# Kernel tuning notes

Hardware: AMD Instinct MI355X
Metric: run time of the kernel (lower is better)

## Reference

```python
import jax, jax.numpy as jnp
import numpy as np

B, S = 2, 1024
D, L, HD, H, KV, F, E, K, V = 1024, 2, 64, 16, 4, 2048, 8, 2, 32000
EPS = 1e-5
THETA = 1e6
REP = H // KV


def setup_inputs() -> dict:
    key = jax.random.key(0)
    ks = jax.random.split(key, 12)
    w = lambda k, shape: jax.random.normal(k, shape, jnp.float32) * 0.02
    return {
        'input_ids': jax.random.randint(ks[0], (B, S), 0, V, jnp.int32),
        'positions': jnp.arange(S),
        'tok_emb': w(ks[1], (V, D)),
        'attn_norm_w': jnp.ones((L, D), jnp.float32),
        'ffn_norm_w': jnp.ones((L, D), jnp.float32),
        'wq': w(ks[2], (L, D, H * HD)),
        'wk': w(ks[3], (L, D, KV * HD)),
        'wv': w(ks[4], (L, D, KV * HD)),
        'wo': w(ks[5], (L, H * HD, D)),
        'gate_w': w(ks[6], (L, D, E)),
        'w1': w(ks[7], (L, E, D, F)),
        'w2': w(ks[8], (L, E, F, D)),
        'w3': w(ks[9], (L, E, D, F)),
        'final_norm_w': jnp.ones((D,), jnp.float32),
        'out_w': w(ks[10], (D, V)),
    }


def rmsnorm(x, w):
    x32 = x.astype(jnp.float32)
    n = x32 * jax.lax.rsqrt(jnp.mean(x32 * x32, axis=-1, keepdims=True) + EPS)
    return n.astype(x.dtype) * w


def rope(x, cos, sin):
    # x: [B, S, h, HD]; cos/sin: [S, HD//2]; pairs are interleaved (even, odd)
    xe, xo = x[..., 0::2], x[..., 1::2]
    c, s = cos[None, :, None, :], sin[None, :, None, :]
    re = xe * c - xo * s
    im = xe * s + xo * c
    return jnp.stack([re, im], axis=-1).reshape(x.shape)


def attention(x, cos, sin, mask, wq_l, wk_l, wv_l, wo_l):
    q = (x @ wq_l).reshape(B, S, H, HD)
    k = (x @ wk_l).reshape(B, S, KV, HD)
    v = (x @ wv_l).reshape(B, S, KV, HD)
    q, k = rope(q, cos, sin), rope(k, cos, sin)
    k = jnp.repeat(k, REP, axis=2)  # GQA: repeat_interleave kv heads
    v = jnp.repeat(v, REP, axis=2)
    scale = HD ** -0.5
    scores = jnp.einsum('bqhd,bkhd->bhqk', q, k) * scale + mask[None, None]
    p = jax.nn.softmax(scores.astype(jnp.float32), axis=-1).astype(q.dtype)
    o = jnp.einsum('bhqk,bkhd->bqhd', p, v).reshape(B, S, H * HD)
    return o @ wo_l


def moe(x, gate_l, w1_l, w2_l, w3_l):
    xs = x.reshape(-1, D)  # [N, D]
    N = xs.shape[0]
    logits = xs @ gate_l  # [N, E]
    topw, sel = jax.lax.top_k(logits, K)
    topw = jax.nn.softmax(topw.astype(jnp.float32), axis=1).astype(x.dtype)
    comb = jnp.zeros((N, E), x.dtype).at[jnp.arange(N)[:, None], sel].add(topw)
    h1 = jax.nn.silu(jnp.einsum('nd,edf->nef', xs, w1_l))
    h3 = jnp.einsum('nd,edf->nef', xs, w3_l)
    y = jnp.einsum('nef,efd->ned', h1 * h3, w2_l)
    return jnp.einsum('ned,ne->nd', y, comb).reshape(x.shape)


def reference(input_ids, positions, tok_emb, attn_norm_w, ffn_norm_w, wq, wk, wv, wo,
              gate_w, w1, w2, w3, final_norm_w, out_w):
    freqs = 1.0 / (THETA ** (jnp.arange(0, HD, 2, dtype=jnp.float32) / HD))  # [HD//2]
    ang = positions.astype(jnp.float32)[:, None] * freqs[None, :]  # [S, HD//2]
    cos, sin = jnp.cos(ang), jnp.sin(ang)
    mask = jnp.triu(jnp.full((S, S), -1e9, jnp.float32), 1)  # causal
    h = tok_emb[input_ids]  # [B, S, D]
    for l in range(L):
        h = h + attention(rmsnorm(h, attn_norm_w[l]), cos, sin, mask, wq[l], wk[l], wv[l], wo[l])
        h = h + moe(rmsnorm(h, ffn_norm_w[l]), gate_w[l], w1[l], w2[l], w3[l])
    return rmsnorm(h, final_norm_w) @ out_w  # [B, S, V]
```

## Files before the change

kernel.cpp:

```cpp
#include <hip/hip_runtime.h>
#include <math.h>

typedef unsigned short ushort_t;
typedef __attribute__((ext_vector_type(8))) short short8;
typedef __attribute__((ext_vector_type(4))) float f32x4;

#define Bq 2
#define Sq 1024
#define Dq 1024
#define Lq 2
#define HDq 64
#define Hq 16
#define KVq 4
#define Fq 2048
#define Eq 8
#define TOPK 2
#define Vq 32000
#define Nq (Bq*Sq)
#define EPSq 1e-5f
#define MROW (Nq*TOPK)

__device__ __forceinline__ float b2f(ushort_t u) {
  return __uint_as_float(((unsigned int)u) << 16);
}
__device__ __forceinline__ ushort_t f2b(float f) {
  unsigned int u = __float_as_uint(f);
  u += 0x7fffu + ((u >> 16) & 1u);
  return (ushort_t)(u >> 16);
}

typedef const void __attribute__((address_space(1)))* gas_cptr;
typedef void __attribute__((address_space(3)))* las_ptr;
__device__ __forceinline__ void gload16(const void* g, void* l) {
  __builtin_amdgcn_global_load_lds((gas_cptr)g, (las_ptr)l, 16, 0, 0);
}

__device__ __forceinline__ void xcd_tiles(int &bx, int &by) {
  int gx = gridDim.x;
  int nwg = gx * gridDim.y;
  int bid = blockIdx.y * gx + blockIdx.x;
  int q8 = nwg >> 3, r8 = nwg & 7;
  int xcd = bid & 7, idx = bid >> 3;
  int swz = (xcd < r8) ? xcd * (q8 + 1) + idx
                       : r8 * (q8 + 1) + (xcd - r8) * q8 + idx;
  bx = swz % gx;
  by = swz / gx;
}

#define MF ((size_t)1024*1024)
#define O_H    ((size_t)0)
#define O_XH   (2*MF)
#define O_XL   (3*MF)
#define O_QKV  (4*MF)
#define O_ATH  (7*MF)
#define O_ATL  (8*MF)
#define O_QH   (9*MF)
#define O_QL   (10*MF)
#define O_KH   (11*MF)
#define O_KL   (11*MF + MF/4)
#define O_VTH  (11*MF + MF/2)
#define O_VTL  (11*MF + 3*MF/4)
#define O_COS  (12*MF)
#define O_SIN  (O_COS + 32768)
#define O_LOG  (O_SIN + 32768)
#define O_TPW  (O_LOG + 16384)
#define O_WTH  (O_COS + MF/8)
#define O_WTL  (O_WTH + MF/2)
#define O_SC   (27*MF/2)
#define O_XGH  (4*MF)
#define O_XGL  (6*MF)
#define O_HB   (O_SC)
#define O_H13H (O_SC + 16*MF)
#define O_H13L (O_SC + 20*MF)
#define O_Y    (O_SC + 24*MF)
#define O_INT  (42*MF)


__global__ void k_rope_table(const int* __restrict__ pos, float* __restrict__ cosT,
                             float* __restrict__ sinT) {
  int i = blockIdx.x * blockDim.x + threadIdx.x;
  if (i >= Sq * 32) return;
  int s = i >> 5, f = i & 31;
  float freq = 1.0f / powf(1.0e6f, (float)f / 32.0f);
  float ang = (float)pos[s] * freq;
  cosT[i] = cosf(ang);
  sinT[i] = sinf(ang);
}

__global__ void k_embed(const int* __restrict__ ids, const float* __restrict__ emb,
                        float* __restrict__ h) {
  int n = blockIdx.x;
  const float4* src = (const float4*)(emb + (size_t)ids[n] * Dq);
  float4* dst = (float4*)(h + (size_t)n * Dq);
  dst[threadIdx.x] = src[threadIdx.x];
}

__global__ void k_rmsnorm3(const float* __restrict__ in, const float* __restrict__ w,
                           ushort_t* __restrict__ outh, ushort_t* __restrict__ outl) {
  int n = blockIdx.x;
  int t = threadIdx.x;
  float4 v = ((const float4*)(in + (size_t)n * Dq))[t];
  float ss = v.x*v.x + v.y*v.y + v.z*v.z + v.w*v.w;
  #pragma unroll
  for (int o = 32; o > 0; o >>= 1) ss += __shfl_down(ss, o);
  __shared__ float red[4];
  if ((t & 63) == 0) red[t >> 6] = ss;
  __syncthreads();
  float tot = red[0] + red[1] + red[2] + red[3];
  float r = rsqrtf(tot / (float)Dq + EPSq);
  float4 wl = ((const float4*)w)[t];
  float o4[4];
  o4[0] = v.x * r * wl.x; o4[1] = v.y * r * wl.y;
  o4[2] = v.z * r * wl.z; o4[3] = v.w * r * wl.w;
  ushort_t* oh = outh + (size_t)n * Dq + t * 4;
  ushort_t* ol = outl + (size_t)n * Dq + t * 4;
  #pragma unroll
  for (int j = 0; j < 4; j++) {
    ushort_t hi = f2b(o4[j]);
    oh[j] = hi;
    ol[j] = f2b(o4[j] - b2f(hi));
  }
}

__global__ void k_rope3(const float* __restrict__ qkv, const float* __restrict__ cosT,
                        const float* __restrict__ sinT,
                        ushort_t* __restrict__ qh, ushort_t* __restrict__ ql,
                        ushort_t* __restrict__ kh, ushort_t* __restrict__ kl) {
  int i = blockIdx.x * blockDim.x + threadIdx.x;
  int n = i / 640, r = i % 640;
  int hh = r >> 5, f = r & 31;
  int s = n & (Sq - 1);
  float c = cosT[s * 32 + f], sn = sinT[s * 32 + f];
  int srcCol = (hh < 16) ? hh * 64 + 2 * f : 1024 + (hh - 16) * 64 + 2 * f;
  const float* pp = qkv + (size_t)n * 1536 + srcCol;
  float xe = pp[0], xo = pp[1];
  float re = xe * c - xo * sn;
  float im = xe * sn + xo * c;
  ushort_t reh = f2b(re), imh = f2b(im);
  ushort_t rel = f2b(re - b2f(reh)), iml = f2b(im - b2f(imh));
  if (hh < 16) {
    size_t d = (size_t)n * 1024 + hh * 64 + 2 * f;
    qh[d] = reh; qh[d + 1] = imh;
    ql[d] = rel; ql[d + 1] = iml;
  } else {
    size_t d = (size_t)n * 256 + (hh - 16) * 64 + 2 * f;
    kh[d] = reh; kh[d + 1] = imh;
    kl[d] = rel; kl[d + 1] = iml;
  }
}

__global__ void k_convT2(const float* __restrict__ src, ushort_t* __restrict__ dh,
                         ushort_t* __restrict__ dl, int srcStride, int dstStride,
                         int zdiv, long long srcZa, long long srcZb, long long dstZ) {
  __shared__ float tile[32][33];
  int z = blockIdx.z;
  const float* s = src + (long long)(z / zdiv) * srcZa + (long long)(z % zdiv) * srcZb;
  int r0 = blockIdx.y * 32, c0 = blockIdx.x * 32;
  int tc = threadIdx.x & 31, tr = threadIdx.x >> 5;
  #pragma unroll
  for (int i = 0; i < 4; ++i)
    tile[tr + i * 8][tc] = s[(long long)(r0 + tr + i * 8) * srcStride + c0 + tc];
  __syncthreads();
  #pragma unroll
  for (int i = 0; i < 4; ++i) {
    float v = tile[tc][tr + i * 8];
    ushort_t hi = f2b(v);
    long long idx = (long long)z * dstZ + (long long)(c0 + tr + i * 8) * dstStride + r0 + tc;
    dh[idx] = hi;
    if (dl) dl[idx] = f2b(v - b2f(hi));
  }
}

__global__ __launch_bounds__(256)
void k_mgemm3(const ushort_t* __restrict__ Ah, const ushort_t* __restrict__ Al,
              const ushort_t* __restrict__ Bh, const ushort_t* __restrict__ Bl,
              float* __restrict__ C,
              int N, int Kd, int lda, int ldc,
              int outmode, int mode,
              const int* __restrict__ grpBase, const int* __restrict__ grpCnt, int M) {
  __shared__ alignas(16) short Ash[128 * 64];
  __shared__ alignas(16) short Asl[128 * 64];
  __shared__ alignas(16) short Bsh[128 * 64];
  __shared__ alignas(16) short Bsl[128 * 64];
  int z = blockIdx.z;
  const ushort_t *Abh, *Abl, *Bbh, *Bbl;
  long long cOff;
  int Me = M;
  if (mode == 1) {
    int base = grpBase[z];
    Me = grpCnt[z];
    Abh = Ah + (long long)base * lda;
    Abl = Al + (long long)base * lda;
    long long bo = (long long)z * ((long long)N * Kd);
    Bbh = Bh + bo; Bbl = Bl + bo;
    cOff = (long long)base * ldc;
  } else {
    Abh = Ah; Abl = Al; Bbh = Bh; Bbl = Bl; cOff = 0;
  }
  int bx, by;
  xcd_tiles(bx, by);
  int m0 = bx * 128, n0 = by * 128;
  if (m0 >= Me) return;
  int t = threadIdx.x, w = t >> 6, lane = t & 63;
  int wm = w >> 1, wn = w & 1;
  int rA = lane >> 3;
  int sOff = ((lane & 7) ^ rA) << 3;
  f32x4 acc[4][4];
  #pragma unroll
  for (int i = 0; i < 4; ++i)
    #pragma unroll
    for (int j = 0; j < 4; ++j) { acc[i][j].x = 0.f; acc[i][j].y = 0.f; acc[i][j].z = 0.f; acc[i][j].w = 0.f; }
  int nkt = Kd >> 6;
  for (int kt = 0; kt < nkt; ++kt) {
    int k0 = kt << 6;
    #pragma unroll
    for (int i = 0; i < 4; ++i) {
      int j = (w << 2) + i;
      int row = (j << 3) + rA;
      long long ao = (long long)(m0 + row) * lda + k0 + sOff;
      long long bo = (long long)(n0 + row) * Kd + k0 + sOff;
      gload16(Abh + ao, &Ash[j * 512]);
      gload16(Abl + ao, &Asl[j * 512]);
      gload16(Bbh + bo, &Bsh[j * 512]);
      gload16(Bbl + bo, &Bsl[j * 512]);
    }
    __syncthreads();
    #pragma unroll
    for (int kk = 0; kk < 2; ++kk) {
      short8 afh[4], afl[4], bfh[4], bfl[4];
      int cl = (kk << 2) + (lane >> 4);
      #pragma unroll
      for (int mi = 0; mi < 4; ++mi) {
        int row = (wm << 6) + (mi << 4) + (lane & 15);
        int idx = (row << 6) + ((cl ^ (row & 7)) << 3);
        afh[mi] = *(const short8*)&Ash[idx];
        afl[mi] = *(const short8*)&Asl[idx];
      }
      #pragma unroll
      for (int nj = 0; nj < 4; ++nj) {
        int row = (wn << 6) + (nj << 4) + (lane & 15);
        int idx = (row << 6) + ((cl ^ (row & 7)) << 3);
        bfh[nj] = *(const short8*)&Bsh[idx];
        bfl[nj] = *(const short8*)&Bsl[idx];
      }
      #pragma unroll
      for (int mi = 0; mi < 4; ++mi)
        #pragma unroll
        for (int nj = 0; nj < 4; ++nj) {
          acc[mi][nj] = __builtin_amdgcn_mfma_f32_16x16x32_bf16(afh[mi], bfh[nj], acc[mi][nj], 0, 0, 0);
          acc[mi][nj] = __builtin_amdgcn_mfma_f32_16x16x32_bf16(afl[mi], bfh[nj], acc[mi][nj], 0, 0, 0);
          acc[mi][nj] = __builtin_amdgcn_mfma_f32_16x16x32_bf16(afh[mi], bfl[nj], acc[mi][nj], 0, 0, 0);
        }
    }
    __syncthreads();
  }
  #pragma unroll
  for (int mi = 0; mi < 4; ++mi) {
    #pragma unroll
    for (int nj = 0; nj < 4; ++nj) {
      int col = n0 + (wn << 6) + (nj << 4) + (lane & 15);
      if (col >= N) continue;
      #pragma unroll
      for (int r = 0; r < 4; ++r) {
        int lr = m0 + (wm << 6) + (mi << 4) + (lane >> 4) * 4 + r;
        if (lr >= Me) continue;
        long long ci = cOff + (long long)lr * ldc + col;
        float v = ((float*)&acc[mi][nj])[r];
        if (outmode == 0) C[ci] = v;
        else C[ci] += v;
      }
    }
  }
}

__global__ __launch_bounds__(256)
void k_mgemm1(const ushort_t* __restrict__ Ah, const ushort_t* __restrict__ Bh,
              float* __restrict__ C,
              int N, int Kd, int lda, int ldc,
              int outmode, int mode,
              const int* __restrict__ grpBase, const int* __restrict__ grpCnt, int M) {
  __shared__ alignas(16) short Ash[2][128 * 64];
  __shared__ alignas(16) short Bsh[2][128 * 64];
  int z = blockIdx.z;
  const ushort_t *Abh, *Bbh;
  long long cOff;
  int Me = M;
  if (mode == 1) {
    int base = grpBase[z];
    Me = grpCnt[z];
    Abh = Ah + (long long)base * lda;
    Bbh = Bh + (long long)z * ((long long)N * Kd);
    cOff = (long long)base * ldc;
  } else {
    Abh = Ah; Bbh = Bh; cOff = 0;
  }
  int bx, by;
  xcd_tiles(bx, by);
  int m0 = bx * 128, n0 = by * 128;
  if (m0 >= Me) return;
  int t = threadIdx.x, w = t >> 6, lane = t & 63;
  int wm = w >> 1, wn = w & 1;
  int rA = lane >> 3;
  int sOff = ((lane & 7) ^ rA) << 3;
  f32x4 acc[4][4];
  #pragma unroll
  for (int i = 0; i < 4; ++i)
    #pragma unroll
    for (int j = 0; j < 4; ++j) { acc[i][j].x = 0.f; acc[i][j].y = 0.f; acc[i][j].z = 0.f; acc[i][j].w = 0.f; }
  int nkt = Kd >> 6;
  #pragma unroll
  for (int i = 0; i < 4; ++i) {
    int j = (w << 2) + i;
    int row = (j << 3) + rA;
    gload16(Abh + (long long)(m0 + row) * lda + sOff, &Ash[0][j * 512]);
    gload16(Bbh + (long long)(n0 + row) * Kd + sOff, &Bsh[0][j * 512]);
  }
  __syncthreads();
  int cur = 0;
  for (int kt = 0; kt < nkt; ++kt) {
    if (kt + 1 < nkt) {
      int k0 = (kt + 1) << 6;
      #pragma unroll
      for (int i = 0; i < 4; ++i) {
        int j = (w << 2) + i;
        int row = (j << 3) + rA;
        gload16(Abh + (long long)(m0 + row) * lda + k0 + sOff, &Ash[cur ^ 1][j * 512]);
        gload16(Bbh + (long long)(n0 + row) * Kd + k0 + sOff, &Bsh[cur ^ 1][j * 512]);
      }
    }
    #pragma unroll
    for (int kk = 0; kk < 2; ++kk) {
      short8 afh[4], bfh[4];
      int cl = (kk << 2) + (lane >> 4);
      #pragma unroll
      for (int mi = 0; mi < 4; ++mi) {
        int row = (wm << 6) + (mi << 4) + (lane & 15);
        afh[mi] = *(const short8*)&Ash[cur][(row << 6) + ((cl ^ (row & 7)) << 3)];
      }
      #pragma unroll
      for (int nj = 0; nj < 4; ++nj) {
        int row = (wn << 6) + (nj << 4) + (lane & 15);
        bfh[nj] = *(const short8*)&Bsh[cur][(row << 6) + ((cl ^ (row & 7)) << 3)];
      }
      #pragma unroll
      for (int mi = 0; mi < 4; ++mi)
        #pragma unroll
        for (int nj = 0; nj < 4; ++nj)
          acc[mi][nj] = __builtin_amdgcn_mfma_f32_16x16x32_bf16(afh[mi], bfh[nj], acc[mi][nj], 0, 0, 0);
    }
    __syncthreads();
    cur ^= 1;
  }
  #pragma unroll
  for (int mi = 0; mi < 4; ++mi) {
    #pragma unroll
    for (int nj = 0; nj < 4; ++nj) {
      int col = n0 + (wn << 6) + (nj << 4) + (lane & 15);
      if (col >= N) continue;
      #pragma unroll
      for (int r = 0; r < 4; ++r) {
        int lr = m0 + (wm << 6) + (mi << 4) + (lane >> 4) * 4 + r;
        if (lr >= Me) continue;
        long long ci = cOff + (long long)lr * ldc + col;
        float v = ((float*)&acc[mi][nj])[r];
        if (outmode == 0) C[ci] = v;
        else C[ci] += v;
      }
    }
  }
}

__global__ __launch_bounds__(256)
void k_qk3(const ushort_t* __restrict__ qh, const ushort_t* __restrict__ ql,
           const ushort_t* __restrict__ kh, const ushort_t* __restrict__ kl,
           float* __restrict__ sc) {
  __shared__ alignas(16) short Ash[128 * 64];
  __shared__ alignas(16) short Asl[128 * 64];
  __shared__ alignas(16) short Bsh[128 * 64];
  __shared__ alignas(16) short Bsl[128 * 64];
  int zl = blockIdx.z;
  int b = zl >> 4, hh = zl & 15, kv = hh >> 2;
  int m0 = blockIdx.x * 128, n0 = blockIdx.y * 128;
  if (n0 > m0 + 127) return;
  long long aBase = ((long long)(b * Sq) * Hq + hh) * HDq;
  long long bBase = ((long long)(b * Sq) * KVq + kv) * HDq;
  int t = threadIdx.x, w = t >> 6, lane = t & 63;
  int wm = w >> 1, wn = w & 1;
  int rA = lane >> 3;
  int sOff = ((lane & 7) ^ rA) << 3;
  f32x4 acc[4][4];
  #pragma unroll
  for (int i = 0; i < 4; ++i)
    #pragma unroll
    for (int j = 0; j < 4; ++j) { acc[i][j].x = 0.f; acc[i][j].y = 0.f; acc[i][j].z = 0.f; acc[i][j].w = 0.f; }
  {
    #pragma unroll
    for (int i = 0; i < 4; ++i) {
      int j = (w << 2) + i;
      int row = (j << 3) + rA;
      long long ao = aBase + (long long)(m0 + row) * (Hq * HDq) + sOff;
      long long bo = bBase + (long long)(n0 + row) * (KVq * HDq) + sOff;
      gload16(qh + ao, &Ash[j * 512]);
      gload16(ql + ao, &Asl[j * 512]);
      gload16(kh + bo, &Bsh[j * 512]);
      gload16(kl + bo, &Bsl[j * 512]);
    }
    __syncthreads();
    #pragma unroll
    for (int kk = 0; kk < 2; ++kk) {
      short8 afh[4], afl[4], bfh[4], bfl[4];
      int cl = (kk << 2) + (lane >> 4);
      #pragma unroll
      for (int mi = 0; mi < 4; ++mi) {
        int row = (wm << 6) + (mi << 4) + (lane & 15);
        int idx = (row << 6) + ((cl ^ (row & 7)) << 3);
        afh[mi] = *(const short8*)&Ash[idx];
        afl[mi] = *(const short8*)&Asl[idx];
      }
      #pragma unroll
      for (int nj = 0; nj < 4; ++nj) {
        int row = (wn << 6) + (nj << 4) + (lane & 15);
        int idx = (row << 6) + ((cl ^ (row & 7)) << 3);
        bfh[nj] = *(const short8*)&Bsh[idx];
        bfl[nj] = *(const short8*)&Bsl[idx];
      }
      #pragma unroll
      for (int mi = 0; mi < 4; ++mi)
        #pragma unroll
        for (int nj = 0; nj < 4; ++nj) {
          acc[mi][nj] = __builtin_amdgcn_mfma_f32_16x16x32_bf16(afh[mi], bfh[nj], acc[mi][nj], 0, 0, 0);
          acc[mi][nj] = __builtin_amdgcn_mfma_f32_16x16x32_bf16(afl[mi], bfh[nj], acc[mi][nj], 0, 0, 0);
          acc[mi][nj] = __builtin_amdgcn_mfma_f32_16x16x32_bf16(afh[mi], bfl[nj], acc[mi][nj], 0, 0, 0);
        }
    }
  }
  float* out = sc + (long long)zl * Sq * Sq;
  #pragma unroll
  for (int mi = 0; mi < 4; ++mi) {
    #pragma unroll
    for (int nj = 0; nj < 4; ++nj) {
      int col = n0 + (wn << 6) + (nj << 4) + (lane & 15);
      #pragma unroll
      for (int r = 0; r < 4; ++r) {
        int lr = m0 + (wm << 6) + (mi << 4) + (lane >> 4) * 4 + r;
        out[(long long)lr * Sq + col] = ((float*)&acc[mi][nj])[r] * 0.125f;
      }
    }
  }
}

__global__ __launch_bounds__(256)
void k_softmax3(const float* __restrict__ sc, ushort_t* __restrict__ ph,
                ushort_t* __restrict__ pl) {
  int row = blockIdx.x * 4 + (threadIdx.x >> 6);
  int lane = threadIdx.x & 63;
  int qi = row & (Sq - 1);
  const float* p = sc + (long long)row * Sq;
  float vals[16];
  float mx = -3.0e38f;
  #pragma unroll
  for (int j = 0; j < 16; j++) {
    int idx = lane + j * 64;
    float v = (idx <= qi) ? p[idx] : -3.0e38f;
    vals[j] = v;
    mx = fmaxf(mx, v);
  }
  #pragma unroll
  for (int o = 32; o > 0; o >>= 1) mx = fmaxf(mx, __shfl_xor(mx, o));
  float sum = 0.0f;
  #pragma unroll
  for (int j = 0; j < 16; j++) {
    int idx = lane + j * 64;
    float e = (idx <= qi) ? expf(vals[j] - mx) : 0.0f;
    vals[j] = e;
    sum += e;
  }
  #pragma unroll
  for (int o = 32; o > 0; o >>= 1) sum += __shfl_xor(sum, o);
  float inv = 1.0f / sum;
  long long base = (long long)row * Sq;
  #pragma unroll
  for (int j = 0; j < 16; j++) {
    int idx = lane + j * 64;
    float pr = vals[j] * inv;
    ushort_t hi = f2b(pr);
    ph[base + idx] = hi;
    pl[base + idx] = f2b(pr - b2f(hi));
  }
}

__global__ __launch_bounds__(256)
void k_pv3(const ushort_t* __restrict__ ph, const ushort_t* __restrict__ pl,
           const ushort_t* __restrict__ vth, const ushort_t* __restrict__ vtl,
           ushort_t* __restrict__ ath, ushort_t* __restrict__ atl) {
  __shared__ alignas(16) short Ash[128 * 64];
  __shared__ alignas(16) short Asl[128 * 64];
  __shared__ alignas(16) short Bsh[128 * 64];
  __shared__ alignas(16) short Bsl[128 * 64];
  int zl = blockIdx.z;
  int b = zl >> 4, hh = zl & 15, kv = hh >> 2;
  int m0 = blockIdx.x * 128;
  const ushort_t* Abh = ph + (long long)zl * Sq * Sq;
  const ushort_t* Abl = pl + (long long)zl * Sq * Sq;
  const ushort_t* Bbh = vth + (long long)((b * KVq + kv) * HDq) * Sq;
  const ushort_t* Bbl = vtl + (long long)((b * KVq + kv) * HDq) * Sq;
  int t = threadIdx.x, w = t >> 6, lane = t & 63;
  int wm = w >> 1, wn = w & 1;
  int rA = lane >> 3;
  int sOff = ((lane & 7) ^ rA) << 3;
  f32x4 acc[4][4];
  #pragma unroll
  for (int i = 0; i < 4; ++i)
    #pragma unroll
    for (int j = 0; j < 4; ++j) { acc[i][j].x = 0.f; acc[i][j].y = 0.f; acc[i][j].z = 0.f; acc[i][j].w = 0.f; }
  int ktmax = 2 * blockIdx.x + 2;
  for (int kt = 0; kt < ktmax; ++kt) {
    int k0 = kt << 6;
    #pragma unroll
    for (int i = 0; i < 4; ++i) {
      int j = (w << 2) + i;
      int row = (j << 3) + rA;
      long long ao = (long long)(m0 + row) * Sq + k0 + sOff;
      long long bo = (long long)(row & 63) * Sq + k0 + sOff;
      gload16(Abh + ao, &Ash[j * 512]);
      gload16(Abl + ao, &Asl[j * 512]);
      gload16(Bbh + bo, &Bsh[j * 512]);
      gload16(Bbl + bo, &Bsl[j * 512]);
    }
    __syncthreads();
    #pragma unroll
    for (int kk = 0; kk < 2; ++kk) {
      short8 afh[4], afl[4], bfh[4], bfl[4];
      int cl = (kk << 2) + (lane >> 4);
      #pragma unroll
      for (int mi = 0; mi < 4; ++mi) {
        int row = (wm << 6) + (mi << 4) + (lane & 15);
        int idx = (row << 6) + ((cl ^ (row & 7)) << 3);
        afh[mi] = *(const short8*)&Ash[idx];
        afl[mi] = *(const short8*)&Asl[idx];
      }
      #pragma unroll
      for (int nj = 0; nj < 4; ++nj) {
        int row = (wn << 6) + (nj << 4) + (lane & 15);
        int idx = (row << 6) + ((cl ^ (row & 7)) << 3);
        bfh[nj] = *(const short8*)&Bsh[idx];
        bfl[nj] = *(const short8*)&Bsl[idx];
      }
      #pragma unroll
      for (int mi = 0; mi < 4; ++mi)
        #pragma unroll
        for (int nj = 0; nj < 4; ++nj) {
          acc[mi][nj] = __builtin_amdgcn_mfma_f32_16x16x32_bf16(afh[mi], bfh[nj], acc[mi][nj], 0, 0, 0);
          acc[mi][nj] = __builtin_amdgcn_mfma_f32_16x16x32_bf16(afl[mi], bfh[nj], acc[mi][nj], 0, 0, 0);
          acc[mi][nj] = __builtin_amdgcn_mfma_f32_16x16x32_bf16(afh[mi], bfl[nj], acc[mi][nj], 0, 0, 0);
        }
    }
    __syncthreads();
  }
  #pragma unroll
  for (int mi = 0; mi < 4; ++mi) {
    #pragma unroll
    for (int nj = 0; nj < 4; ++nj) {
      int col = (wn << 6) + (nj << 4) + (lane & 15);
      if (col >= HDq) continue;
      #pragma unroll
      for (int r = 0; r < 4; ++r) {
        int lr = m0 + (wm << 6) + (mi << 4) + (lane >> 4) * 4 + r;
        long long ci = ((long long)(b * Sq + lr)) * (Hq * HDq) + hh * HDq + col;
        float v = ((float*)&acc[mi][nj])[r];
        ushort_t hi = f2b(v);
        ath[ci] = hi;
        atl[ci] = f2b(v - b2f(hi));
      }
    }
  }
}

__global__ void k_gate(const ushort_t* __restrict__ xh, const ushort_t* __restrict__ xl,
                       const float* __restrict__ gw, float* __restrict__ logits) {
  int n = blockIdx.x * 4 + (threadIdx.x >> 6);
  int lane = threadIdx.x & 63;
  float acc[Eq];
  #pragma unroll
  for (int e = 0; e < Eq; e++) acc[e] = 0.0f;
  for (int d = lane; d < Dq; d += 64) {
    size_t idx = (size_t)n * Dq + d;
    float xv = b2f(xh[idx]) + b2f(xl[idx]);
    const float* g = gw + (size_t)d * Eq;
    #pragma unroll
    for (int e = 0; e < Eq; e++) acc[e] += xv * g[e];
  }
  #pragma unroll
  for (int o = 32; o > 0; o >>= 1)
    #pragma unroll
    for (int e = 0; e < Eq; e++) acc[e] += __shfl_xor(acc[e], o);
  if (lane == 0) {
    #pragma unroll
    for (int e = 0; e < Eq; e++) logits[(size_t)n * Eq + e] = acc[e];
  }
}

__global__ void k_zero_counts(int* c) { if (threadIdx.x < 16) c[threadIdx.x] = 0; }

__global__ void k_route_count(const float* __restrict__ logits, float* __restrict__ topw,
                              int* __restrict__ sel, int* __restrict__ counts) {
  int n = blockIdx.x * blockDim.x + threadIdx.x;
  if (n >= Nq) return;
  const float* lg = logits + (size_t)n * Eq;
  int i1 = 0; float v1 = lg[0];
  #pragma unroll
  for (int e = 1; e < Eq; e++) if (lg[e] > v1) { v1 = lg[e]; i1 = e; }
  int i2 = -1; float v2 = -3.0e38f;
  #pragma unroll
  for (int e = 0; e < Eq; e++) if (e != i1 && lg[e] > v2) { v2 = lg[e]; i2 = e; }
  float e2 = expf(v2 - v1);
  float s = 1.0f + e2;
  topw[n * 2 + 0] = 1.0f / s;
  topw[n * 2 + 1] = e2 / s;
  sel[n * 2 + 0] = i1;
  sel[n * 2 + 1] = i2;
  atomicAdd(&counts[i1], 1);
  atomicAdd(&counts[i2], 1);
}

__global__ void k_scan(const int* __restrict__ counts, int* __restrict__ bases,
                       int* __restrict__ counts2) {
  if (threadIdx.x == 0) {
    int s = 0;
    for (int e = 0; e < Eq; e++) { bases[e] = s; s += counts[e]; counts2[e] = 0; }
  }
}

__global__ void k_route_assign(const int* __restrict__ sel, int* __restrict__ counts2,
                               const int* __restrict__ bases, int* __restrict__ row2tok,
                               int* __restrict__ posof) {
  int n = blockIdx.x * blockDim.x + threadIdx.x;
  if (n >= Nq) return;
  #pragma unroll
  for (int slot = 0; slot < TOPK; slot++) {
    int e = sel[n * 2 + slot];
    int pos = atomicAdd(&counts2[e], 1);
    int row = bases[e] + pos;
    row2tok[row] = n;
    posof[n * 2 + slot] = row;
  }
}

__global__ void k_gather_us(const ushort_t* __restrict__ xh, const ushort_t* __restrict__ xl,
                            const int* __restrict__ row2tok,
                            ushort_t* __restrict__ xgh, ushort_t* __restrict__ xgl) {
  int row = blockIdx.x;
  int tok = row2tok[row];
  int t = threadIdx.x;
  const uint2* sh = (const uint2*)(xh + (size_t)tok * Dq);
  const uint2* sl = (const uint2*)(xl + (size_t)tok * Dq);
  ((uint2*)(xgh + (size_t)row * Dq))[t] = sh[t];
  ((uint2*)(xgl + (size_t)row * Dq))[t] = sl[t];
}

__global__ void k_silumul3b(const float* __restrict__ hb,
                            ushort_t* __restrict__ oh, ushort_t* __restrict__ ol) {
  long total = (long)MROW * Fq;
  long i = (long)blockIdx.x * blockDim.x + threadIdx.x;
  long st = (long)gridDim.x * blockDim.x;
  for (; i < total; i += st) {
    long r = i >> 11, f = i & 2047;
    float a = hb[(r << 12) + f];
    float b = hb[(r << 12) + 2048 + f];
    float s = (a / (1.0f + expf(-a))) * b;
    ushort_t hi = f2b(s);
    oh[i] = hi;
    ol[i] = f2b(s - b2f(hi));
  }
}

__global__ void k_moe_combine(float* __restrict__ h, const float* __restrict__ y,
                              const float* __restrict__ topw, const int* __restrict__ posof) {
  int n = blockIdx.x;
  int t = threadIdx.x;
  float w0 = topw[n * 2 + 0], w1 = topw[n * 2 + 1];
  int r0 = posof[n * 2 + 0], r1 = posof[n * 2 + 1];
  float4 a = ((const float4*)(y + (size_t)r0 * Dq))[t];
  float4 b = ((const float4*)(y + (size_t)r1 * Dq))[t];
  float4 hv = ((float4*)(h + (size_t)n * Dq))[t];
  hv.x += w0 * a.x + w1 * b.x;
  hv.y += w0 * a.y + w1 * b.y;
  hv.z += w0 * a.z + w1 * b.z;
  hv.w += w0 * a.w + w1 * b.w;
  ((float4*)(h + (size_t)n * Dq))[t] = hv;
}

extern "C" void kernel_launch(void* const* d_in, const int* in_sizes, int n_in,
                              void* d_out, int out_size, void* d_ws, size_t ws_size,
                              hipStream_t stream) {
  const int* ids       = (const int*)d_in[0];
  const int* pos       = (const int*)d_in[1];
  const float* tok_emb = (const float*)d_in[2];
  const float* attn_nw = (const float*)d_in[3];
  const float* ffn_nw  = (const float*)d_in[4];
  const float* wq      = (const float*)d_in[5];
  const float* wk      = (const float*)d_in[6];
  const float* wv      = (const float*)d_in[7];
  const float* wo      = (const float*)d_in[8];
  const float* gate    = (const float*)d_in[9];
  const float* w1      = (const float*)d_in[10];
  const float* w2      = (const float*)d_in[11];
  const float* w3      = (const float*)d_in[12];
  const float* fnw     = (const float*)d_in[13];
  const float* outw    = (const float*)d_in[14];
  float* out = (float*)d_out;
  float* ws = (float*)d_ws;
  float* dws = out;

  float* h      = ws + O_H;
  ushort_t* xh  = (ushort_t*)(ws + O_XH);
  ushort_t* xl  = (ushort_t*)(ws + O_XL);
  float* qkv    = ws + O_QKV;
  ushort_t* ath = (ushort_t*)(ws + O_ATH);
  ushort_t* atl = (ushort_t*)(ws + O_ATL);
  ushort_t* qhB = (ushort_t*)(ws + O_QH);
  ushort_t* qlB = (ushort_t*)(ws + O_QL);
  ushort_t* khB = (ushort_t*)(ws + O_KH);
  ushort_t* klB = (ushort_t*)(ws + O_KL);
  ushort_t* vth = (ushort_t*)(ws + O_VTH);
  ushort_t* vtl = (ushort_t*)(ws + O_VTL);
  float* cosT   = ws + O_COS;
  float* sinT   = ws + O_SIN;
  float* logits = ws + O_LOG;
  float* topw   = ws + O_TPW;
  ushort_t* wTh = (ushort_t*)(ws + O_WTH);
  ushort_t* wTl = (ushort_t*)(ws + O_WTL);
  float* sc     = dws;
  ushort_t* ph  = (ushort_t*)(dws + 32*MF);
  ushort_t* pl  = (ushort_t*)(ws + O_SC);
  ushort_t* wQh = (ushort_t*)dws;
  ushort_t* wQl = (ushort_t*)(dws + MF);
  ushort_t* xgh = (ushort_t*)(ws + O_XGH);
  ushort_t* xgl = (ushort_t*)(ws + O_XGL);
  ushort_t* wAh = (ushort_t*)dws;
  ushort_t* wAl = (ushort_t*)(dws + 16*MF);
  float* hb     = ws + O_HB;
  ushort_t* h13h= (ushort_t*)(ws + O_H13H);
  ushort_t* h13l= (ushort_t*)(ws + O_H13L);
  float* y      = ws + O_Y;
  ushort_t* owTh= (ushort_t*)(ws + O_SC);
  int* ip = (int*)(ws + O_INT);
  int* counts  = ip;
  int* counts2 = ip + 8;
  int* bases   = ip + 16;
  int* sel     = ip + 32;
  int* row2tok = ip + 32 + 4096;
  int* posof   = ip + 32 + 8192;

  k_rope_table<<<128, 256, 0, stream>>>(pos, cosT, sinT);
  k_embed<<<Nq, 256, 0, stream>>>(ids, tok_emb, h);

  for (int l = 0; l < Lq; l++) {
    k_rmsnorm3<<<Nq, 256, 0, stream>>>(h, attn_nw + (size_t)l * Dq, xh, xl);
    k_convT2<<<dim3(32, 32, 1), 256, 0, stream>>>(wq + (long long)l*Dq*Hq*HDq, wQh, wQl, Hq*HDq, Dq, 1, 0, 0, 0);
    k_convT2<<<dim3(8, 32, 1), 256, 0, stream>>>(wk + (long long)l*Dq*KVq*HDq, wQh + (size_t)1024*1024, wQl + (size_t)1024*1024, KVq*HDq, Dq, 1, 0, 0, 0);
    k_convT2<<<dim3(8, 32, 1), 256, 0, stream>>>(wv + (long long)l*Dq*KVq*HDq, wQh + (size_t)1280*1024, wQl + (size_t)1280*1024, KVq*HDq, Dq, 1, 0, 0, 0);
    k_mgemm3<<<dim3(16, 12, 1), 256, 0, stream>>>(xh, xl, wQh, wQl, qkv, 1536, Dq, Dq, 1536, 0, 0, nullptr, nullptr, Nq);
    k_rope3<<<(Nq * 20 * 32) / 256, 256, 0, stream>>>(qkv, cosT, sinT, qhB, qlB, khB, klB);
    k_convT2<<<dim3(2, 32, Bq*KVq), 256, 0, stream>>>(qkv + 1280, vth, vtl, 1536, Sq,
           KVq, (long long)Sq*1536, HDq, (long long)HDq*Sq);
    k_qk3<<<dim3(8, 8, 32), 256, 0, stream>>>(qhB, qlB, khB, klB, sc);
    k_softmax3<<<(32 * Sq) / 4, 256, 0, stream>>>(sc, ph, pl);
    k_pv3<<<dim3(8, 1, 32), 256, 0, stream>>>(ph, pl, vth, vtl, ath, atl);
    k_convT2<<<dim3(32, 32, 1), 256, 0, stream>>>(wo + (long long)l*Hq*HDq*Dq, wTh, wTl, Dq, Hq*HDq, 1, 0, 0, 0);
    k_mgemm3<<<dim3(16, 8, 1), 256, 0, stream>>>(ath, atl, wTh, wTl, h, Dq, Hq*HDq, Hq*HDq, Dq, 1, 0, nullptr, nullptr, Nq);

    k_rmsnorm3<<<Nq, 256, 0, stream>>>(h, ffn_nw + (size_t)l * Dq, xh, xl);
    k_gate<<<Nq / 4, 256, 0, stream>>>(xh, xl, gate + (size_t)l * Dq * Eq, logits);
    k_zero_counts<<<1, 32, 0, stream>>>(counts);
    k_route_count<<<Nq / 256, 256, 0, stream>>>(logits, topw, sel, counts);
    k_scan<<<1, 1, 0, stream>>>(counts, bases, counts2);
    k_route_assign<<<Nq / 256, 256, 0, stream>>>(sel, counts2, bases, row2tok, posof);
    k_gather_us<<<MROW, 256, 0, stream>>>(xh, xl, row2tok, xgh, xgl);
    int last = (l == Lq - 1);
    k_convT2<<<dim3(64, 32, 8), 256, 0, stream>>>(w1 + (long long)l*Eq*Dq*Fq, wAh, last ? nullptr : wAl,
           Fq, Dq, 1, (long long)Dq*Fq, 0, (long long)4096*1024);
    k_convT2<<<dim3(64, 32, 8), 256, 0, stream>>>(w3 + (long long)l*Eq*Dq*Fq,
           wAh + (size_t)2048*1024, last ? nullptr : (wAl + (size_t)2048*1024),
           Fq, Dq, 1, (long long)Dq*Fq, 0, (long long)4096*1024);
    if (last) k_mgemm1<<<dim3(16, 32, 8), 256, 0, stream>>>(xgh, wAh, hb, 4096, Dq, Dq, 4096, 0, 1, bases, counts, 0);
    else      k_mgemm3<<<dim3(16, 32, 8), 256, 0, stream>>>(xgh, xgl, wAh, wAl, hb, 4096, Dq, Dq, 4096, 0, 1, bases, counts, 0);
    k_silumul3b<<<4096, 256, 0, stream>>>(hb, h13h, h13l);
    k_convT2<<<dim3(32, 64, 8), 256, 0, stream>>>(w2 + (long long)l*Eq*Fq*Dq, wAh, last ? nullptr : wAl,
           Dq, Fq, 1, (long long)Fq*Dq, 0, (long long)Dq*Fq);
    if (last) k_mgemm1<<<dim3(16, 8, 8), 256, 0, stream>>>(h13h, wAh, y, Dq, Fq, Fq, Dq, 0, 1, bases, counts, 0);
    else      k_mgemm3<<<dim3(16, 8, 8), 256, 0, stream>>>(h13h, h13l, wAh, wAl, y, Dq, Fq, Fq, Dq, 0, 1, bases, counts, 0);
    k_moe_combine<<<Nq, 256, 0, stream>>>(h, y, topw, posof);
  }

  k_rmsnorm3<<<Nq, 256, 0, stream>>>(h, fnw, xh, xl);
  k_convT2<<<dim3(1000, 32, 1), 256, 0, stream>>>(outw, owTh, nullptr, Vq, Dq, 1, 0, 0, 0);
  k_mgemm1<<<dim3(16, 250, 1), 256, 0, stream>>>(xh, owTh, out, Vq, Dq, Dq, Vq, 0, 0, nullptr, nullptr, Nq);
}
```

Measured before the change: 1.451 ms.

## Fuse SiLU-gate multiply into MoE up-projection epilogue and double-buffer PV kernel

The w1 and w3 weights are interleaved row-wise during transposition, so each adjacent output column pair holds the gate and up values. The grouped GEMM epilogue then uses a lane shuffle to compute silu(a)*b and writes the bf16 hi/lo split directly. This removes the fp32 intermediate buffer and the separate silumul kernel. Separately, the attention PV kernel gains double-buffered shared-memory tile loads to overlap global loads with MFMA work, at the cost of twice the LDS use, which may lower occupancy.

```diff
diff --git a/kernel.cpp b/kernel.cpp
--- a/kernel.cpp
+++ b/kernel.cpp
@@ -69,7 +69,6 @@
 #define O_SC   (27*MF/2)
 #define O_XGH  (4*MF)
 #define O_XGL  (6*MF)
-#define O_HB   (O_SC)
 #define O_H13H (O_SC + 16*MF)
 #define O_H13L (O_SC + 20*MF)
 #define O_Y    (O_SC + 24*MF)
@@ -151,7 +150,8 @@
 
 __global__ void k_convT2(const float* __restrict__ src, ushort_t* __restrict__ dh,
                          ushort_t* __restrict__ dl, int srcStride, int dstStride,
-                         int zdiv, long long srcZa, long long srcZb, long long dstZ) {
+                         int zdiv, long long srcZa, long long srcZb, long long dstZ,
+                         int rowScale, int rowOff) {
   __shared__ float tile[32][33];
   int z = blockIdx.z;
   const float* s = src + (long long)(z / zdiv) * srcZa + (long long)(z % zdiv) * srcZb;
@@ -165,7 +165,8 @@
   for (int i = 0; i < 4; ++i) {
     float v = tile[tc][tr + i * 8];
     ushort_t hi = f2b(v);
-    long long idx = (long long)z * dstZ + (long long)(c0 + tr + i * 8) * dstStride + r0 + tc;
+    long long drow = (long long)(c0 + tr + i * 8) * rowScale + rowOff;
+    long long idx = (long long)z * dstZ + drow * dstStride + r0 + tc;
     dh[idx] = hi;
     if (dl) dl[idx] = f2b(v - b2f(hi));
   }
@@ -175,6 +176,7 @@
 void k_mgemm3(const ushort_t* __restrict__ Ah, const ushort_t* __restrict__ Al,
               const ushort_t* __restrict__ Bh, const ushort_t* __restrict__ Bl,
               float* __restrict__ C,
+              ushort_t* __restrict__ Ch2, ushort_t* __restrict__ Cl2,
               int N, int Kd, int lda, int ldc,
               int outmode, int mode,
               const int* __restrict__ grpBase, const int* __restrict__ grpCnt, int M) {
@@ -184,7 +186,7 @@
   __shared__ alignas(16) short Bsl[128 * 64];
   int z = blockIdx.z;
   const ushort_t *Abh, *Abl, *Bbh, *Bbl;
-  long long cOff;
+  long long cOff, cOff2;
   int Me = M;
   if (mode == 1) {
     int base = grpBase[z];
@@ -194,8 +196,9 @@
     long long bo = (long long)z * ((long long)N * Kd);
     Bbh = Bh + bo; Bbl = Bl + bo;
     cOff = (long long)base * ldc;
+    cOff2 = (long long)base * 2048;
   } else {
-    Abh = Ah; Abl = Al; Bbh = Bh; Bbl = Bl; cOff = 0;
+    Abh = Ah; Abl = Al; Bbh = Bh; Bbl = Bl; cOff = 0; cOff2 = 0;
   }
   int bx, by;
   xcd_tiles(bx, by);
@@ -259,15 +262,21 @@
     #pragma unroll
     for (int nj = 0; nj < 4; ++nj) {
       int col = n0 + (wn << 6) + (nj << 4) + (lane & 15);
-      if (col >= N) continue;
       #pragma unroll
       for (int r = 0; r < 4; ++r) {
         int lr = m0 + (wm << 6) + (mi << 4) + (lane >> 4) * 4 + r;
-        if (lr >= Me) continue;
-        long long ci = cOff + (long long)lr * ldc + col;
         float v = ((float*)&acc[mi][nj])[r];
-        if (outmode == 0) C[ci] = v;
-        else C[ci] += v;
+        float pv = __shfl_xor(v, 1);
+        if (col >= N || lr >= Me) continue;
+        if (outmode == 0) C[cOff + (long long)lr * ldc + col] = v;
+        else if (outmode == 1) C[cOff + (long long)lr * ldc + col] += v;
+        else if (!(lane & 1)) {
+          float s = (v / (1.0f + expf(-v))) * pv;
+          long long ci2 = cOff2 + (long long)lr * 2048 + (col >> 1);
+          ushort_t hi = f2b(s);
+          Ch2[ci2] = hi;
+          Cl2[ci2] = f2b(s - b2f(hi));
+        }
       }
     }
   }
@@ -276,6 +285,7 @@
 __global__ __launch_bounds__(256)
 void k_mgemm1(const ushort_t* __restrict__ Ah, const ushort_t* __restrict__ Bh,
               float* __restrict__ C,
+              ushort_t* __restrict__ Ch2, ushort_t* __restrict__ Cl2,
               int N, int Kd, int lda, int ldc,
               int outmode, int mode,
               const int* __restrict__ grpBase, const int* __restrict__ grpCnt, int M) {
@@ -283,7 +293,7 @@
   __shared__ alignas(16) short Bsh[2][128 * 64];
   int z = blockIdx.z;
   const ushort_t *Abh, *Bbh;
-  long long cOff;
+  long long cOff, cOff2;
   int Me = M;
   if (mode == 1) {
     int base = grpBase[z];
@@ -291,8 +301,9 @@
     Abh = Ah + (long long)base * lda;
     Bbh = Bh + (long long)z * ((long long)N * Kd);
     cOff = (long long)base * ldc;
+    cOff2 = (long long)base * 2048;
   } else {
-    Abh = Ah; Bbh = Bh; cOff = 0;
+    Abh = Ah; Bbh = Bh; cOff = 0; cOff2 = 0;
   }
   int bx, by;
   xcd_tiles(bx, by);
@@ -356,15 +367,21 @@
     #pragma unroll
     for (int nj = 0; nj < 4; ++nj) {
       int col = n0 + (wn << 6) + (nj << 4) + (lane & 15);
-      if (col >= N) continue;
       #pragma unroll
       for (int r = 0; r < 4; ++r) {
         int lr = m0 + (wm << 6) + (mi << 4) + (lane >> 4) * 4 + r;
-        if (lr >= Me) continue;
-        long long ci = cOff + (long long)lr * ldc + col;
         float v = ((float*)&acc[mi][nj])[r];
-        if (outmode == 0) C[ci] = v;
-        else C[ci] += v;
+        float pv = __shfl_xor(v, 1);
+        if (col >= N || lr >= Me) continue;
+        if (outmode == 0) C[cOff + (long long)lr * ldc + col] = v;
+        else if (outmode == 1) C[cOff + (long long)lr * ldc + col] += v;
+        else if (!(lane & 1)) {
+          float s = (v / (1.0f + expf(-v))) * pv;
+          long long ci2 = cOff2 + (long long)lr * 2048 + (col >> 1);
+          ushort_t hi = f2b(s);
+          Ch2[ci2] = hi;
+          Cl2[ci2] = f2b(s - b2f(hi));
+        }
       }
     }
   }
@@ -493,10 +510,10 @@
 void k_pv3(const ushort_t* __restrict__ ph, const ushort_t* __restrict__ pl,
            const ushort_t* __restrict__ vth, const ushort_t* __restrict__ vtl,
            ushort_t* __restrict__ ath, ushort_t* __restrict__ atl) {
-  __shared__ alignas(16) short Ash[128 * 64];
-  __shared__ alignas(16) short Asl[128 * 64];
-  __shared__ alignas(16) short Bsh[128 * 64];
-  __shared__ alignas(16) short Bsl[128 * 64];
+  __shared__ alignas(16) short Ash[2][128 * 64];
+  __shared__ alignas(16) short Asl[2][128 * 64];
+  __shared__ alignas(16) short Bsh[2][128 * 64];
+  __shared__ alignas(16) short Bsl[2][128 * 64];
   int zl = blockIdx.z;
   int b = zl >> 4, hh = zl & 15, kv = hh >> 2;
   int m0 = blockIdx.x * 128;
@@ -514,20 +531,34 @@
     #pragma unroll
     for (int j = 0; j < 4; ++j) { acc[i][j].x = 0.f; acc[i][j].y = 0.f; acc[i][j].z = 0.f; acc[i][j].w = 0.f; }
   int ktmax = 2 * blockIdx.x + 2;
+  #pragma unroll
+  for (int i = 0; i < 4; ++i) {
+    int j = (w << 2) + i;
+    int row = (j << 3) + rA;
+    long long ao = (long long)(m0 + row) * Sq + sOff;
+    long long bo = (long long)(row & 63) * Sq + sOff;
+    gload16(Abh + ao, &Ash[0][j * 512]);
+    gload16(Abl + ao, &Asl[0][j * 512]);
+    gload16(Bbh + bo, &Bsh[0][j * 512]);
+    gload16(Bbl + bo, &Bsl[0][j * 512]);
+  }
+  __syncthreads();
+  int cur = 0;
   for (int kt = 0; kt < ktmax; ++kt) {
-    int k0 = kt << 6;
-    #pragma unroll
-    for (int i = 0; i < 4; ++i) {
-      int j = (w << 2) + i;
-      int row = (j << 3) + rA;
-      long long ao = (long long)(m0 + row) * Sq + k0 + sOff;
-      long long bo = (long long)(row & 63) * Sq + k0 + sOff;
-      gload16(Abh + ao, &Ash[j * 512]);
-      gload16(Abl + ao, &Asl[j * 512]);
-      gload16(Bbh + bo, &Bsh[j * 512]);
-      gload16(Bbl + bo, &Bsl[j * 512]);
-    }
-    __syncthreads();
+    if (kt + 1 < ktmax) {
+      int k0 = (kt + 1) << 6;
+      #pragma unroll
+      for (int i = 0; i < 4; ++i) {
+        int j = (w << 2) + i;
+        int row = (j << 3) + rA;
+        long long ao = (long long)(m0 + row) * Sq + k0 + sOff;
+        long long bo = (long long)(row & 63) * Sq + k0 + sOff;
+        gload16(Abh + ao, &Ash[cur ^ 1][j * 512]);
+        gload16(Abl + ao, &Asl[cur ^ 1][j * 512]);
+        gload16(Bbh + bo, &Bsh[cur ^ 1][j * 512]);
+        gload16(Bbl + bo, &Bsl[cur ^ 1][j * 512]);
+      }
+    }
     #pragma unroll
     for (int kk = 0; kk < 2; ++kk) {
       short8 afh[4], afl[4], bfh[4], bfl[4];
@@ -536,15 +567,15 @@
       for (int mi = 0; mi < 4; ++mi) {
         int row = (wm << 6) + (mi << 4) + (lane & 15);
         int idx = (row << 6) + ((cl ^ (row & 7)) << 3);
-        afh[mi] = *(const short8*)&Ash[idx];
-        afl[mi] = *(const short8*)&Asl[idx];
+        afh[mi] = *(const short8*)&Ash[cur][idx];
+        afl[mi] = *(const short8*)&Asl[cur][idx];
       }
       #pragma unroll
       for (int nj = 0; nj < 4; ++nj) {
         int row = (wn << 6) + (nj << 4) + (lane & 15);
         int idx = (row << 6) + ((cl ^ (row & 7)) << 3);
-        bfh[nj] = *(const short8*)&Bsh[idx];
-        bfl[nj] = *(const short8*)&Bsl[idx];
+        bfh[nj] = *(const short8*)&Bsh[cur][idx];
+        bfl[nj] = *(const short8*)&Bsl[cur][idx];
       }
       #pragma unroll
       for (int mi = 0; mi < 4; ++mi)
@@ -556,6 +587,7 @@
         }
     }
     __syncthreads();
+    cur ^= 1;
   }
   #pragma unroll
   for (int mi = 0; mi < 4; ++mi) {
@@ -656,22 +688,6 @@
   const uint2* sl = (const uint2*)(xl + (size_t)tok * Dq);
   ((uint2*)(xgh + (size_t)row * Dq))[t] = sh[t];
   ((uint2*)(xgl + (size_t)row * Dq))[t] = sl[t];
-}
-
-__global__ void k_silumul3b(const float* __restrict__ hb,
-                            ushort_t* __restrict__ oh, ushort_t* __restrict__ ol) {
-  long total = (long)MROW * Fq;
-  long i = (long)blockIdx.x * blockDim.x + threadIdx.x;
-  long st = (long)gridDim.x * blockDim.x;
-  for (; i < total; i += st) {
-    long r = i >> 11, f = i & 2047;
-    float a = hb[(r << 12) + f];
-    float b = hb[(r << 12) + 2048 + f];
-    float s = (a / (1.0f + expf(-a))) * b;
-    ushort_t hi = f2b(s);
-    oh[i] = hi;
-    ol[i] = f2b(s - b2f(hi));
-  }
 }
 
 __global__ void k_moe_combine(float* __restrict__ h, const float* __restrict__ y,
@@ -739,7 +755,6 @@
   ushort_t* xgl = (ushort_t*)(ws + O_XGL);
   ushort_t* wAh = (ushort_t*)dws;
   ushort_t* wAl = (ushort_t*)(dws + 16*MF);
-  float* hb     = ws + O_HB;
   ushort_t* h13h= (ushort_t*)(ws + O_H13H);
   ushort_t* h13l= (ushort_t*)(ws + O_H13L);
   float* y      = ws + O_Y;
@@ -757,18 +772,18 @@
 
   for (int l = 0; l < Lq; l++) {
     k_rmsnorm3<<<Nq, 256, 0, stream>>>(h, attn_nw + (size_t)l * Dq, xh, xl);
-    k_convT2<<<dim3(32, 32, 1), 256, 0, stream>>>(wq + (long long)l*Dq*Hq*HDq, wQh, wQl, Hq*HDq, Dq, 1, 0, 0, 0);
-    k_convT2<<<dim3(8, 32, 1), 256, 0, stream>>>(wk + (long long)l*Dq*KVq*HDq, wQh + (size_t)1024*1024, wQl + (size_t)1024*1024, KVq*HDq, Dq, 1, 0, 0, 0);
-    k_convT2<<<dim3(8, 32, 1), 256, 0, stream>>>(wv + (long long)l*Dq*KVq*HDq, wQh + (size_t)1280*1024, wQl + (size_t)1280*1024, KVq*HDq, Dq, 1, 0, 0, 0);
-    k_mgemm3<<<dim3(16, 12, 1), 256, 0, stream>>>(xh, xl, wQh, wQl, qkv, 1536, Dq, Dq, 1536, 0, 0, nullptr, nullptr, Nq);
+    k_convT2<<<dim3(32, 32, 1), 256, 0, stream>>>(wq + (long long)l*Dq*Hq*HDq, wQh, wQl, Hq*HDq, Dq, 1, 0, 0, 0, 1, 0);
+    k_convT2<<<dim3(8, 32, 1), 256, 0, stream>>>(wk + (long long)l*Dq*KVq*HDq, wQh + (size_t)1024*1024, wQl + (size_t)1024*1024, KVq*HDq, Dq, 1, 0, 0, 0, 1, 0);
+    k_convT2<<<dim3(8, 32, 1), 256, 0, stream>>>(wv + (long long)l*Dq*KVq*HDq, wQh + (size_t)1280*1024, wQl + (size_t)1280*1024, KVq*HDq, Dq, 1, 0, 0, 0, 1, 0);
+    k_mgemm3<<<dim3(16, 12, 1), 256, 0, stream>>>(xh, xl, wQh, wQl, qkv, nullptr, nullptr, 1536, Dq, Dq, 1536, 0, 0, nullptr, nullptr, Nq);
     k_rope3<<<(Nq * 20 * 32) / 256, 256, 0, stream>>>(qkv, cosT, sinT, qhB, qlB, khB, klB);
     k_convT2<<<dim3(2, 32, Bq*KVq), 256, 0, stream>>>(qkv + 1280, vth, vtl, 1536, Sq,
-           KVq, (long long)Sq*1536, HDq, (long long)HDq*Sq);
+           KVq, (long long)Sq*1536, HDq, (long long)HDq*Sq, 1, 0);
     k_qk3<<<dim3(8, 8, 32), 256, 0, stream>>>(qhB, qlB, khB, klB, sc);
     k_softmax3<<<(32 * Sq) / 4, 256, 0, stream>>>(sc, ph, pl);
     k_pv3<<<dim3(8, 1, 32), 256, 0, stream>>>(ph, pl, vth, vtl, ath, atl);
-    k_convT2<<<dim3(32, 32, 1), 256, 0, stream>>>(wo + (long long)l*Hq*HDq*Dq, wTh, wTl, Dq, Hq*HDq, 1, 0, 0, 0);
-    k_mgemm3<<<dim3(16, 8, 1), 256, 0, stream>>>(ath, atl, wTh, wTl, h, Dq, Hq*HDq, Hq*HDq, Dq, 1, 0, nullptr, nullptr, Nq);
+    k_convT2<<<dim3(32, 32, 1), 256, 0, stream>>>(wo + (long long)l*Hq*HDq*Dq, wTh, wTl, Dq, Hq*HDq, 1, 0, 0, 0, 1, 0);
+    k_mgemm3<<<dim3(16, 8, 1), 256, 0, stream>>>(ath, atl, wTh, wTl, h, nullptr, nullptr, Dq, Hq*HDq, Hq*HDq, Dq, 1, 0, nullptr, nullptr, Nq);
 
     k_rmsnorm3<<<Nq, 256, 0, stream>>>(h, ffn_nw + (size_t)l * Dq, xh, xl);
     k_gate<<<Nq / 4, 256, 0, stream>>>(xh, xl, gate + (size_t)l * Dq * Eq, logits);
@@ -779,21 +794,19 @@
     k_gather_us<<<MROW, 256, 0, stream>>>(xh, xl, row2tok, xgh, xgl);
     int last = (l == Lq - 1);
     k_convT2<<<dim3(64, 32, 8), 256, 0, stream>>>(w1 + (long long)l*Eq*Dq*Fq, wAh, last ? nullptr : wAl,
-           Fq, Dq, 1, (long long)Dq*Fq, 0, (long long)4096*1024);
-    k_convT2<<<dim3(64, 32, 8), 256, 0, stream>>>(w3 + (long long)l*Eq*Dq*Fq,
-           wAh + (size_t)2048*1024, last ? nullptr : (wAl + (size_t)2048*1024),
-           Fq, Dq, 1, (long long)Dq*Fq, 0, (long long)4096*1024);
-    if (last) k_mgemm1<<<dim3(16, 32, 8), 256, 0, stream>>>(xgh, wAh, hb, 4096, Dq, Dq, 4096, 0, 1, bases, counts, 0);
-    else      k_mgemm3<<<dim3(16, 32, 8), 256, 0, stream>>>(xgh, xgl, wAh, wAl, hb, 4096, Dq, Dq, 4096, 0, 1, bases, counts, 0);
-    k_silumul3b<<<4096, 256, 0, stream>>>(hb, h13h, h13l);
+           Fq, Dq, 1, (long long)Dq*Fq, 0, (long long)4096*1024, 2, 0);
+    k_convT2<<<dim3(64, 32, 8), 256, 0, stream>>>(w3 + (long long)l*Eq*Dq*Fq, wAh, last ? nullptr : wAl,
+           Fq, Dq, 1, (long long)Dq*Fq, 0, (long long)4096*1024, 2, 1);
+    if (last) k_mgemm1<<<dim3(16, 32, 8), 256, 0, stream>>>(xgh, wAh, nullptr, h13h, h13l, 4096, Dq, Dq, 4096, 2, 1, bases, counts, 0);
+    else      k_mgemm3<<<dim3(16, 32, 8), 256, 0, stream>>>(xgh, xgl, wAh, wAl, nullptr, h13h, h13l, 4096, Dq, Dq, 4096, 2, 1, bases, counts, 0);
     k_convT2<<<dim3(32, 64, 8), 256, 0, stream>>>(w2 + (long long)l*Eq*Fq*Dq, wAh, last ? nullptr : wAl,
-           Dq, Fq, 1, (long long)Fq*Dq, 0, (long long)Dq*Fq);
-    if (last) k_mgemm1<<<dim3(16, 8, 8), 256, 0, stream>>>(h13h, wAh, y, Dq, Fq, Fq, Dq, 0, 1, bases, counts, 0);
-    else      k_mgemm3<<<dim3(16, 8, 8), 256, 0, stream>>>(h13h, h13l, wAh, wAl, y, Dq, Fq, Fq, Dq, 0, 1, bases, counts, 0);
+           Dq, Fq, 1, (long long)Fq*Dq, 0, (long long)Dq*Fq, 1, 0);
+    if (last) k_mgemm1<<<dim3(16, 8, 8), 256, 0, stream>>>(h13h, wAh, y, nullptr, nullptr, Dq, Fq, Fq, Dq, 0, 1, bases, counts, 0);
+    else      k_mgemm3<<<dim3(16, 8, 8), 256, 0, stream>>>(h13h, h13l, wAh, wAl, y, nullptr, nullptr, Dq, Fq, Fq, Dq, 0, 1, bases, counts, 0);
     k_moe_combine<<<Nq, 256, 0, stream>>>(h, y, topw, posof);
   }
 
   k_rmsnorm3<<<Nq, 256, 0, stream>>>(h, fnw, xh, xl);
-  k_convT2<<<dim3(1000, 32, 1), 256, 0, stream>>>(outw, owTh, nullptr, Vq, Dq, 1, 0, 0, 0);
-  k_mgemm1<<<dim3(16, 250, 1), 256, 0, stream>>>(xh, owTh, out, Vq, Dq, Dq, Vq, 0, 0, nullptr, nullptr, Nq);
-}
+  k_convT2<<<dim3(1000, 32, 1), 256, 0, stream>>>(outw, owTh, nullptr, Vq, Dq, 1, 0, 0, 0, 1, 0);
+  k_mgemm1<<<dim3(16, 250, 1), 256, 0, stream>>>(xh, owTh, out, nullptr, nullptr, Vq, Dq, Dq, Vq, 0, 0, nullptr, nullptr, Nq);
+}
```

New measurement: 1.669 ms. +15.1%, slower.
